# Performance work log

Measured on AMD Instinct MI355X. Metric: run time of the kernel, lower is better.

Reference implementation:

```python
import jax, jax.numpy as jnp
import numpy as np
from jax.experimental.ode import odeint

TOL = 1.0  # ODEBlock default: rtol = atol = tol


def _odefunc(x, t, W1, b1, W2, b2):
    # time-concat MLP: f(x, t) = tanh([x, t] @ W1 + b1) @ W2 + b2
    tcol = jnp.full((x.shape[0], 1), t, dtype=x.dtype)  # [B, 1]
    h = jnp.tanh(jnp.concatenate([x, tcol], axis=1) @ W1 + b1)  # [B, H]
    return h @ W2 + b2  # [B, D]


def setup_inputs() -> dict:
    key = jax.random.key(0)
    k1, k2, k3 = jax.random.split(key, 3)
    B, D, H = 4096, 2048, 2048
    # scale weights so the dynamics stay well-conditioned over t in [0,1]
    x = jax.random.normal(k1, (B, D), dtype=jnp.float32)
    W1 = jax.random.normal(k2, (D + 1, H), dtype=jnp.float32) / np.sqrt(D + 1)
    b1 = jnp.zeros((H,), dtype=jnp.float32)
    W2 = jax.random.normal(k3, (H, D), dtype=jnp.float32) / np.sqrt(H)
    b2 = jnp.zeros((D,), dtype=jnp.float32)
    return {"x": x, "W1": W1, "b1": b1, "W2": W2, "b2": b2}


def reference(x, W1, b1, W2, b2):
    f = lambda y, t: _odefunc(y, t, W1, b1, W2, b2)
    ts = jnp.array([0.0, 1.0], dtype=jnp.float32)
    states = odeint(f, x, ts, rtol=TOL, atol=TOL)  # [2, B, D]
    return states[-1]
```

## Files before the change

kernel.cpp:

```cpp
#include <hip/hip_runtime.h>

typedef unsigned short u16;
typedef __attribute__((ext_vector_type(8))) short short8;
typedef __attribute__((ext_vector_type(4))) float floatx4;

#define BD 4096
#define DD 2048
#define NTOT (BD*DD)
#define MAX_STEPS 3

#define CE0 ((float)(35.0/384.0 - 1951.0/21600.0))
#define CE2 ((float)(500.0/1113.0 - 22642.0/50085.0))
#define CE3 ((float)(125.0/192.0 - 451.0/720.0))
#define CE4 ((float)(-2187.0/6784.0 + 12231.0/42400.0))
#define CE5 ((float)(11.0/84.0 - 649.0/6300.0))
#define CE6 ((float)(-1.0/60.0))

#define CM0 ((float)(6025192743.0/30085553152.0/2.0))
#define CM2 ((float)(51252292925.0/65400821598.0/2.0))
#define CM3 ((float)(-2691868925.0/45128329728.0/2.0))
#define CM4 ((float)(187940372067.0/1594534317056.0/2.0))
#define CM5 ((float)(-1776094331.0/19743644256.0/2.0))
#define CM6 ((float)(11237099.0/235043384.0/2.0))

#define CS0 ((float)(35.0/384.0))
#define CS2 ((float)(500.0/1113.0))
#define CS3 ((float)(125.0/192.0))
#define CS4 ((float)(-2187.0/6784.0))
#define CS5 ((float)(11.0/84.0))

#define B50 ((float)(9017.0/3168.0))
#define B51 ((float)(-355.0/33.0))
#define B52 ((float)(46732.0/5247.0))
#define B53 ((float)(49.0/176.0))
#define B54 ((float)(-5103.0/18656.0))

struct Scal {
  float t, dt, last_t, h0, dt_saved;
  float d0s, d1s, d2s, errs;
  float d0, d1;
  int run_flag, accept_flag, cur;
};

__device__ __forceinline__ u16 f2bf(float x) {
  unsigned int u = __float_as_uint(x);
  u += 0x7FFFu + ((u >> 16) & 1u);
  return (u16)(u >> 16);
}
__device__ __forceinline__ float bf2f(u16 h) {
  return __uint_as_float(((unsigned int)h) << 16);
}
__device__ __forceinline__ void splitw(float v, u16* oh, u16* ol, size_t idx) {
  u16 h = f2bf(v);
  oh[idx] = h;
  ol[idx] = f2bf(v - bf2f(h));
}

__device__ __forceinline__ void gload16(const u16* g, u16* l) {
  __builtin_amdgcn_global_load_lds(
      (const __attribute__((address_space(1))) void*)g,
      (__attribute__((address_space(3))) void*)l, 16, 0, 0);
}

__global__ void transpose_hi(const float* __restrict__ W, u16* __restrict__ th,
                             int K, int N) {
  __shared__ float tile[32][33];
  int k0 = blockIdx.x * 32, n0 = blockIdx.y * 32;
  int tx = threadIdx.x, ty = threadIdx.y;
  #pragma unroll
  for (int j = 0; j < 32; j += 8)
    tile[ty + j][tx] = W[(size_t)(k0 + ty + j) * N + n0 + tx];
  __syncthreads();
  #pragma unroll
  for (int j = 0; j < 32; j += 8) {
    int nn = ty + j, kk = tx;
    th[(size_t)(n0 + nn) * K + k0 + kk] = f2bf(tile[kk][nn]);
  }
}

template <int STAGE>
__global__ __launch_bounds__(256, 4)
void gemm_fused(const u16* __restrict__ Ah, const u16* __restrict__ Al,
                const u16* __restrict__ Bt,
                const float* __restrict__ bias, const float* __restrict__ trow,
                int tmode, float alpha_c,
                float bb0, float bb1, float bb2, float bbv,
                float* __restrict__ YA, float* __restrict__ YB,
                float* __restrict__ F,
                float* __restrict__ K2M, float* __restrict__ K3,
                float* __restrict__ K4,
                u16* __restrict__ oh, u16* __restrict__ ol,
                Scal* __restrict__ s, int flag) {
  if (flag == 1 && !s->run_flag) return;

  __shared__ __attribute__((aligned(16))) u16 lAh[64 * 64];
  __shared__ __attribute__((aligned(16))) u16 lAl[64 * 64];
  __shared__ __attribute__((aligned(16))) u16 lB[128 * 64];

  const int tid = threadIdx.x;
  const int lane = tid & 63;
  const int wave = tid >> 6;

  const int lin = blockIdx.x;
  const int xcd = lin & 7;
  const int slot = lin >> 3;
  const int bm = (xcd * 8 + (slot >> 4)) * 64;
  const int bn = (slot & 15) * 128;

  const int m_w = (wave >> 1) * 32;
  const int n_w = (wave & 1) * 64;
  const int lr = lane & 15;

  const int lrow = lane >> 3;
  const int lcol = (((lane & 7) ^ (lane >> 3)) << 3);
  const int ra = wave * 16;
  const int rb = wave * 32;
  const u16* gAh = Ah + (size_t)(bm + ra + lrow) * DD + lcol;
  const u16* gAl = Al + (size_t)(bm + ra + lrow) * DD + lcol;
  const u16* gB  = Bt + (size_t)(bn + rb + lrow) * DD + lcol;
  u16* dAh = &lAh[ra * 64];
  u16* dAl = &lAl[ra * 64];
  u16* dB  = &lB[rb * 64];

  floatx4 acc[2][4];
  #pragma unroll
  for (int i = 0; i < 2; ++i)
    #pragma unroll
    for (int j = 0; j < 4; ++j)
      acc[i][j] = (floatx4){0.f, 0.f, 0.f, 0.f};

  for (int k0 = 0; k0 < DD; k0 += 64) {
    if (k0) __syncthreads();
    #pragma unroll
    for (int t = 0; t < 2; ++t) {
      gload16(gAh + k0 + (size_t)(8 * t) * DD, dAh + (8 * t) * 64);
      gload16(gAl + k0 + (size_t)(8 * t) * DD, dAl + (8 * t) * 64);
    }
    #pragma unroll
    for (int t = 0; t < 4; ++t)
      gload16(gB + k0 + (size_t)(8 * t) * DD, dB + (8 * t) * 64);
    __syncthreads();

    #pragma unroll
    for (int kk = 0; kk < 2; ++kk) {
      const int cb = kk * 4 + (lane >> 4);
      short8 afh[2], afl[2], bfv[4];
      #pragma unroll
      for (int i = 0; i < 2; ++i) {
        int r = m_w + i * 16 + lr;
        int ar = r * 64 + ((cb ^ (lr & 7)) << 3);
        afh[i] = *(const short8*)&lAh[ar];
        afl[i] = *(const short8*)&lAl[ar];
      }
      #pragma unroll
      for (int j = 0; j < 4; ++j) {
        int r = n_w + j * 16 + lr;
        bfv[j] = *(const short8*)&lB[r * 64 + ((cb ^ (lr & 7)) << 3)];
      }
      #pragma unroll
      for (int i = 0; i < 2; ++i)
        #pragma unroll
        for (int j = 0; j < 4; ++j) {
          acc[i][j] = __builtin_amdgcn_mfma_f32_16x16x32_bf16(afh[i], bfv[j], acc[i][j], 0, 0, 0);
          acc[i][j] = __builtin_amdgcn_mfma_f32_16x16x32_bf16(afl[i], bfv[j], acc[i][j], 0, 0, 0);
        }
    }
  }

  const int cur = s->cur;
  const float* Yc = cur ? YB : YA;
  float* NY = cur ? YA : YB;
  const float dt = s->dt;
  float tj = 0.f;
  if (STAGE == 100) tj = (tmode == 0) ? (s->t + dt * alpha_c) : s->h0;

  float err_acc = 0.f;
  const int oq = (lane >> 4) * 4;
  const int oc = lane & 15;
  #pragma unroll
  for (int i = 0; i < 2; ++i)
    #pragma unroll
    for (int j = 0; j < 4; ++j)
      #pragma unroll
      for (int r = 0; r < 4; ++r) {
        int m = bm + m_w + i * 16 + oq + r;
        int n = bn + n_w + j * 16 + oc;
        float v = acc[i][j][r] + bias[n];
        size_t idx = (size_t)m * DD + n;
        if constexpr (STAGE == 100) {
          float h = tanhf(v + tj * trow[n]);
          splitw(h, oh, ol, idx);
        } else if constexpr (STAGE == 0) {
          float fv = F[idx];
          float yv = Yc[idx];
          K2M[idx] = v;
          float ys = yv + dt * (bb0 * fv + bbv * v);
          splitw(ys, oh, ol, idx);
        } else if constexpr (STAGE == 1) {
          float fv = F[idx];
          float yv = Yc[idx];
          float k2v = K2M[idx];
          K3[idx] = v;
          float ys = yv + dt * (bb0 * fv + bb1 * k2v + bbv * v);
          splitw(ys, oh, ol, idx);
        } else if constexpr (STAGE == 2) {
          float fv = F[idx];
          float yv = Yc[idx];
          float k2v = K2M[idx];
          float k3v = K3[idx];
          K4[idx] = v;
          float ys = yv + dt * (bb0 * fv + bb1 * k2v + bb2 * k3v + bbv * v);
          splitw(ys, oh, ol, idx);
        } else if constexpr (STAGE == 3) {
          float fv = F[idx], yv = Yc[idx];
          float k2v = K2M[idx], k3v = K3[idx], k4v = K4[idx];
          K2M[idx] = v;
          float ys = yv + dt * (B50 * fv + B51 * k2v + B52 * k3v + B53 * k4v + B54 * v);
          splitw(ys, oh, ol, idx);
        } else if constexpr (STAGE == 4) {
          float fv = F[idx], yv = Yc[idx];
          float k3v = K3[idx], k4v = K4[idx], k5v = K2M[idx];
          float ny = yv + dt * (CS0 * fv + CS2 * k3v + CS3 * k4v + CS4 * k5v + CS5 * v);
          NY[idx] = ny;
          K3[idx]  = CE0 * fv + CE2 * k3v + CE3 * k4v + CE4 * k5v + CE5 * v;
          K2M[idx] = CM0 * fv + CM2 * k3v + CM3 * k4v + CM4 * k5v + CM5 * v;
          splitw(ny, oh, ol, idx);
        } else if constexpr (STAGE == 5) {
          float Ef = K3[idx] + CE6 * v;
          K3[idx] = Ef;
          K2M[idx] += CM6 * v;
          K4[idx] = v;
          float yv = Yc[idx], nyv = NY[idx];
          float e = dt * Ef;
          float tol = 1.f + fmaxf(fabsf(yv), fabsf(nyv));
          float rr = e / tol;
          err_acc += rr * rr;
        } else if constexpr (STAGE == 10) {
          F[idx] = v;
        } else {
          K4[idx] = v;
        }
      }

  if constexpr (STAGE == 5) {
    __syncthreads();
    float* red = (float*)lAh;
    red[tid] = err_acc;
    __syncthreads();
    for (int off = 128; off > 0; off >>= 1) {
      if (tid < off) red[tid] += red[tid + off];
      __syncthreads();
    }
    if (tid == 0) atomicAdd(&s->errs, red[0]);
  }
}

__global__ void k_init_scal(Scal* s) {
  s->t = 0.f; s->dt = 0.f; s->last_t = 0.f; s->h0 = 0.f; s->dt_saved = 1.f;
  s->d0s = 0.f; s->d1s = 0.f; s->d2s = 0.f; s->errs = 0.f;
  s->d0 = 0.f; s->d1 = 0.f;
  s->run_flag = 0; s->accept_flag = 0; s->cur = 0;
}

__global__ void k_init_y(const float* __restrict__ x, float* __restrict__ y,
                         u16* __restrict__ ysh, u16* __restrict__ ysl, int n) {
  for (int i = blockIdx.x * blockDim.x + threadIdx.x; i < n; i += gridDim.x * blockDim.x) {
    float v = x[i];
    y[i] = v;
    splitw(v, ysh, ysl, i);
  }
}

__global__ void k_probe_ys(const float* __restrict__ y, const float* __restrict__ f,
                           u16* __restrict__ ysh, u16* __restrict__ ysl, int n,
                           const Scal* __restrict__ s) {
  float h0 = s->h0;
  for (int i = blockIdx.x * blockDim.x + threadIdx.x; i < n; i += gridDim.x * blockDim.x)
    splitw(y[i] + h0 * f[i], ysh, ysl, i);
}

__global__ void k_prep(float* YA, float* YB, float* __restrict__ F,
                       float* __restrict__ K3p, const float* __restrict__ K4p,
                       float* __restrict__ K2M,
                       u16* __restrict__ ysh, u16* __restrict__ ysl, int n,
                       const Scal* __restrict__ s, int mode) {
  if (mode == 0 && !s->run_flag) return;
  int acc = (mode == 0) ? s->accept_flag : 0;
  int cur = s->cur;
  const float* Yc = cur ? YB : YA;
  const float* Yn = cur ? YA : YB;
  float dtn = s->dt, dts = s->dt_saved;
  for (int i = blockIdx.x * blockDim.x + threadIdx.x; i < n; i += gridDim.x * blockDim.x) {
    float fold = F[i];
    float fnew, ynext;
    if (acc) {
      fnew = K4p[i];
      ynext = Yn[i];
      F[i] = fnew;
      K3p[i] = fold;
      K2M[i] = Yc[i] + dts * K2M[i];
    } else {
      fnew = fold;
      ynext = Yc[i];
    }
    splitw(ynext + dtn * 0.2f * fnew, ysh, ysl, i);
  }
}

__global__ void k_d01(const float* __restrict__ y, const float* __restrict__ f,
                      int n, Scal* s) {
  float a0 = 0.f, a1 = 0.f;
  for (int i = blockIdx.x * blockDim.x + threadIdx.x; i < n; i += gridDim.x * blockDim.x) {
    float yv = y[i], fv = f[i];
    float sc = 1.f + fabsf(yv);
    float t0 = yv / sc, t1 = fv / sc;
    a0 += t0 * t0;
    a1 += t1 * t1;
  }
  __shared__ float r0[256], r1[256];
  int tid = threadIdx.x;
  r0[tid] = a0; r1[tid] = a1;
  __syncthreads();
  for (int off = 128; off > 0; off >>= 1) {
    if (tid < off) { r0[tid] += r0[tid + off]; r1[tid] += r1[tid + off]; }
    __syncthreads();
  }
  if (tid == 0) { atomicAdd(&s->d0s, r0[0]); atomicAdd(&s->d1s, r1[0]); }
}

__global__ void k_h0(Scal* s) {
  float d0 = sqrtf(s->d0s);
  float d1 = sqrtf(s->d1s);
  s->d0 = d0; s->d1 = d1;
  s->h0 = (d0 < 1e-5f || d1 < 1e-5f) ? 1e-6f : 0.01f * d0 / d1;
}

__global__ void k_d2(const float* __restrict__ y, const float* __restrict__ f,
                     const float* __restrict__ f1h, int n, Scal* s) {
  float a = 0.f;
  for (int i = blockIdx.x * blockDim.x + threadIdx.x; i < n; i += gridDim.x * blockDim.x) {
    float v = (f1h[i] - f[i]) / (1.f + fabsf(y[i]));
    a += v * v;
  }
  __shared__ float r0[256];
  int tid = threadIdx.x;
  r0[tid] = a;
  __syncthreads();
  for (int off = 128; off > 0; off >>= 1) {
    if (tid < off) r0[tid] += r0[tid + off];
    __syncthreads();
  }
  if (tid == 0) atomicAdd(&s->d2s, r0[0]);
}

__global__ void k_dt(Scal* s) {
  float d2 = sqrtf(s->d2s) / s->h0;
  float h1 = (s->d1 <= 1e-15f && d2 <= 1e-15f)
                 ? fmaxf(1e-6f, s->h0 * 1e-3f)
                 : powf(0.01f / fmaxf(s->d1, d2), 1.0f / 6.0f);
  s->dt = fminf(100.f * s->h0, h1);
  s->t = 0.f;
  s->last_t = 0.f;
}

__global__ void k_step_begin(Scal* s) {
  s->run_flag = (s->t < 1.0f) && (s->dt > 0.f);
  s->accept_flag = 0;
  s->errs = 0.f;
}

__global__ void k_step_end(Scal* s) {
  if (!s->run_flag) { s->accept_flag = 0; return; }
  float ratio = sqrtf(s->errs / (float)NTOT);
  int acc = (ratio <= 1.0f);
  s->accept_flag = acc;
  float dfactor = (ratio < 1.f) ? 1.f : 0.2f;
  float factor = fminf(10.f, fmaxf(0.9f * powf(ratio, -0.2f), dfactor));
  float ndt = (ratio == 0.f) ? s->dt * 10.f : s->dt * factor;
  if (ndt < 0.f) ndt = 0.f;
  if (acc) { s->dt_saved = s->dt; s->last_t = s->t; s->t = s->t + s->dt; }
  s->dt = ndt;
}

__global__ void k_flip(Scal* s) {
  if (s->accept_flag) s->cur ^= 1;
}

__global__ void k_final(const float* YA, const float* YB,
    const float* __restrict__ f0s, const float* __restrict__ f1s,
    float* out, int n, const Scal* s) {
  int cur = s->cur;
  const float* y1s = cur ? YB : YA;
  const float* y0s = cur ? YA : YB;
  float dt = s->dt_saved;
  float r = (1.0f - s->last_t) / (s->t - s->last_t);
  for (int i = blockIdx.x * blockDim.x + threadIdx.x; i < n; i += gridDim.x * blockDim.x) {
    float y0 = y0s[i], y1 = y1s[i], ym = out[i], f0 = f0s[i], f1 = f1s[i];
    float a = 2.f * dt * (f1 - f0) - 8.f * (y1 + y0) + 16.f * ym;
    float b = dt * (5.f * f0 - 3.f * f1) + 18.f * y0 + 14.f * y1 - 32.f * ym;
    float c = dt * (f1 - 4.f * f0) - 11.f * y0 - 5.f * y1 + 16.f * ym;
    float d = dt * f0;
    out[i] = (((a * r + b) * r + c) * r + d) * r + y0;
  }
}

__global__ void k_debug_ws(float* __restrict__ out, int n, float mb) {
  for (int i = blockIdx.x * blockDim.x + threadIdx.x; i < n; i += gridDim.x * blockDim.x)
    out[i] = mb;
}

extern "C" void kernel_launch(void* const* d_in, const int* in_sizes, int n_in,
                              void* d_out, int out_size, void* d_ws, size_t ws_size,
                              hipStream_t stream) {
  const float* x  = (const float*)d_in[0];
  const float* W1 = (const float*)d_in[1];
  const float* b1 = (const float*)d_in[2];
  const float* W2 = (const float*)d_in[3];
  const float* b2 = (const float*)d_in[4];
  float* out = (float*)d_out;
  const float* w1row = W1 + (size_t)2048 * 2048;

  const size_t SZW = (size_t)2048 * 2048 * 2;
  const size_t SZH = (size_t)NTOT * 2;
  const size_t SZF = (size_t)NTOT * 4;
  const size_t NEED = 1024 + 2 * SZW + 4 * SZH + 5 * SZF;

  if (ws_size < NEED) {
    k_debug_ws<<<2048, 256, 0, stream>>>(out, NTOT, (float)(ws_size >> 20));
    return;
  }

  char* base = (char*)d_ws;
  Scal* s = (Scal*)base;
  size_t o = 1024;
  auto take = [&](size_t bytes) { void* p = base + o; o += bytes; return p; };

  u16* W1T = (u16*)take(SZW); u16* W2T = (u16*)take(SZW);
  u16* YSH = (u16*)take(SZH); u16* YSL = (u16*)take(SZH);
  u16* HH  = (u16*)take(SZH); u16* HL  = (u16*)take(SZH);
  float* YA = (float*)take(SZF); float* YB = (float*)take(SZF);
  float* F  = (float*)take(SZF);
  float* K3 = (float*)take(SZF); float* K4 = (float*)take(SZF);
  float* K2M = out;

  const dim3 GG(1024), GB(256);
  const dim3 EG(2048), EB(256);

  #define G1(tmode, alpha, flag) \
    gemm_fused<100><<<GG, GB, 0, stream>>>(YSH, YSL, W1T, b1, w1row, \
        tmode, alpha, 0.f, 0.f, 0.f, 0.f, \
        YA, YB, F, K2M, K3, K4, HH, HL, s, flag)
  #define G2(st, b0, b1c, b2c, bv, flag) \
    gemm_fused<st><<<GG, GB, 0, stream>>>(HH, HL, W2T, b2, nullptr, \
        0, 0.f, b0, b1c, b2c, bv, \
        YA, YB, F, K2M, K3, K4, YSH, YSL, s, flag)

  transpose_hi<<<dim3(64, 64), dim3(32, 8), 0, stream>>>(W1, W1T, 2048, 2048);
  transpose_hi<<<dim3(64, 64), dim3(32, 8), 0, stream>>>(W2, W2T, 2048, 2048);
  k_init_scal<<<1, 1, 0, stream>>>(s);
  k_init_y<<<EG, EB, 0, stream>>>(x, YA, YSH, YSL, NTOT);

  G1(0, 0.f, 0); G2(10, 0.f, 0.f, 0.f, 0.f, 0);
  k_d01<<<1024, 256, 0, stream>>>(YA, F, NTOT, s);
  k_h0<<<1, 1, 0, stream>>>(s);
  k_probe_ys<<<EG, EB, 0, stream>>>(YA, F, YSH, YSL, NTOT, s);
  G1(1, 0.f, 0); G2(11, 0.f, 0.f, 0.f, 0.f, 0);
  k_d2<<<1024, 256, 0, stream>>>(YA, F, K4, NTOT, s);
  k_dt<<<1, 1, 0, stream>>>(s);
  k_prep<<<EG, EB, 0, stream>>>(YA, YB, F, K3, K4, K2M, YSH, YSL, NTOT, s, 1);

  for (int st = 0; st < MAX_STEPS; ++st) {
    k_step_begin<<<1, 1, 0, stream>>>(s);
    G1(0, 0.2f, 1);
    G2(0, (float)(3.0/40.0), 0.f, 0.f, (float)(9.0/40.0), 1);
    G1(0, 0.3f, 1);
    G2(1, (float)(44.0/45.0), (float)(-56.0/15.0), 0.f, (float)(32.0/9.0), 1);
    G1(0, 0.8f, 1);
    G2(2, (float)(19372.0/6561.0), (float)(-25360.0/2187.0),
       (float)(64448.0/6561.0), (float)(-212.0/729.0), 1);
    G1(0, (float)(8.0/9.0), 1);
    G2(3, 0.f, 0.f, 0.f, 0.f, 1);
    G1(0, 1.f, 1);
    G2(4, 0.f, 0.f, 0.f, 0.f, 1);
    G1(0, 1.f, 1);
    G2(5, 0.f, 0.f, 0.f, 0.f, 1);

    k_step_end<<<1, 1, 0, stream>>>(s);
    k_prep<<<EG, EB, 0, stream>>>(YA, YB, F, K3, K4, K2M, YSH, YSL, NTOT, s, 0);
    k_flip<<<1, 1, 0, stream>>>(s);
  }

  k_final<<<EG, EB, 0, stream>>>(YA, YB, K3, F, out, NTOT, s);

  #undef G1
  #undef G2
}
```

Measured before the change: 2.784 ms.

## Double-buffer LDS tiles in fused GEMM to overlap loads with MFMA

```diff
diff --git a/kernel.cpp b/kernel.cpp
--- a/kernel.cpp
+++ b/kernel.cpp
@@ -79,7 +79,7 @@
 }
 
 template <int STAGE>
-__global__ __launch_bounds__(256, 4)
+__global__ __launch_bounds__(256, 2)
 void gemm_fused(const u16* __restrict__ Ah, const u16* __restrict__ Al,
                 const u16* __restrict__ Bt,
                 const float* __restrict__ bias, const float* __restrict__ trow,
@@ -93,9 +93,9 @@
                 Scal* __restrict__ s, int flag) {
   if (flag == 1 && !s->run_flag) return;
 
-  __shared__ __attribute__((aligned(16))) u16 lAh[64 * 64];
-  __shared__ __attribute__((aligned(16))) u16 lAl[64 * 64];
-  __shared__ __attribute__((aligned(16))) u16 lB[128 * 64];
+  __shared__ __attribute__((aligned(16))) u16 lAh[2][64 * 64];
+  __shared__ __attribute__((aligned(16))) u16 lAl[2][64 * 64];
+  __shared__ __attribute__((aligned(16))) u16 lB[2][128 * 64];
 
   const int tid = threadIdx.x;
   const int lane = tid & 63;
@@ -118,9 +118,6 @@
   const u16* gAh = Ah + (size_t)(bm + ra + lrow) * DD + lcol;
   const u16* gAl = Al + (size_t)(bm + ra + lrow) * DD + lcol;
   const u16* gB  = Bt + (size_t)(bn + rb + lrow) * DD + lcol;
-  u16* dAh = &lAh[ra * 64];
-  u16* dAl = &lAl[ra * 64];
-  u16* dB  = &lB[rb * 64];
 
   floatx4 acc[2][4];
   #pragma unroll
@@ -129,17 +126,23 @@
     for (int j = 0; j < 4; ++j)
       acc[i][j] = (floatx4){0.f, 0.f, 0.f, 0.f};
 
-  for (int k0 = 0; k0 < DD; k0 += 64) {
-    if (k0) __syncthreads();
+  auto stage = [&](int k0, int b) {
     #pragma unroll
     for (int t = 0; t < 2; ++t) {
-      gload16(gAh + k0 + (size_t)(8 * t) * DD, dAh + (8 * t) * 64);
-      gload16(gAl + k0 + (size_t)(8 * t) * DD, dAl + (8 * t) * 64);
+      gload16(gAh + k0 + (size_t)(8 * t) * DD, &lAh[b][(ra + 8 * t) * 64]);
+      gload16(gAl + k0 + (size_t)(8 * t) * DD, &lAl[b][(ra + 8 * t) * 64]);
     }
     #pragma unroll
     for (int t = 0; t < 4; ++t)
-      gload16(gB + k0 + (size_t)(8 * t) * DD, dB + (8 * t) * 64);
-    __syncthreads();
+      gload16(gB + k0 + (size_t)(8 * t) * DD, &lB[b][(rb + 8 * t) * 64]);
+  };
+
+  stage(0, 0);
+  __syncthreads();
+
+  int bufc = 0;
+  for (int k0 = 0; k0 < DD; k0 += 64) {
+    if (k0 + 64 < DD) stage(k0 + 64, bufc ^ 1);
 
     #pragma unroll
     for (int kk = 0; kk < 2; ++kk) {
@@ -149,13 +152,13 @@
       for (int i = 0; i < 2; ++i) {
         int r = m_w + i * 16 + lr;
         int ar = r * 64 + ((cb ^ (lr & 7)) << 3);
-        afh[i] = *(const short8*)&lAh[ar];
-        afl[i] = *(const short8*)&lAl[ar];
+        afh[i] = *(const short8*)&lAh[bufc][ar];
+        afl[i] = *(const short8*)&lAl[bufc][ar];
       }
       #pragma unroll
       for (int j = 0; j < 4; ++j) {
         int r = n_w + j * 16 + lr;
-        bfv[j] = *(const short8*)&lB[r * 64 + ((cb ^ (lr & 7)) << 3)];
+        bfv[j] = *(const short8*)&lB[bufc][r * 64 + ((cb ^ (lr & 7)) << 3)];
       }
       #pragma unroll
       for (int i = 0; i < 2; ++i)
@@ -165,6 +168,9 @@
           acc[i][j] = __builtin_amdgcn_mfma_f32_16x16x32_bf16(afl[i], bfv[j], acc[i][j], 0, 0, 0);
         }
     }
+
+    __syncthreads();
+    bufc ^= 1;
   }
 
   const int cur = s->cur;
@@ -244,7 +250,7 @@
 
   if constexpr (STAGE == 5) {
     __syncthreads();
-    float* red = (float*)lAh;
+    float* red = (float*)&lAh[0][0];
     red[tid] = err_acc;
     __syncthreads();
     for (int off = 128; off > 0; off >>= 1) {
```

Result: slower. 2.865 ms (+2.9%).
